# Kernel optimization log

Measured on AMD Instinct MI355X. Metric: run time of the kernel, lower is better.

## Reference

```python
import jax, jax.numpy as jnp
import numpy as np

B, S, IN, OUT = 4, 2048, 4096, 4096


def setup_inputs() -> dict:
    key = jax.random.key(0)
    kx, kw, kb = jax.random.split(key, 3)
    x = jax.random.randint(kx, (B, S, IN), -127, 128, dtype=jnp.int8)
    weight = jax.random.randint(kw, (OUT, IN), -127, 128, dtype=jnp.int8)
    # original module initializes bias to zeros(int32); use random int32 to exercise the add
    bias = jax.random.randint(kb, (1, OUT), -1000, 1000, dtype=jnp.int32)
    return {"x": x, "weight": weight, "bias": bias}


def reference(x, weight, bias):
    x_shape = x.shape
    x2 = x.reshape(-1, x_shape[-1])  # [tokens, IN], int8
    # dot_general with preferred_element_type=int32 -> int8 inputs, int32 accumulate
    y = jax.lax.dot_general(
        x2, weight,
        dimension_numbers=(((1,), (1,)), ((), ())),
        preferred_element_type=jnp.int32,
    )  # [tokens, OUT] int32
    y = y + bias  # broadcast [1, OUT] int32
    return y.reshape(*x_shape[:-1], -1)
```

## Files before the change

### kernel.cpp

```cpp
#include <hip/hip_runtime.h>
#include <stdint.h>

#define M_TOT 8192
#define N_TOT 4096
#define K_TOT 4096

typedef int v4i  __attribute__((ext_vector_type(4)));
typedef int v16i __attribute__((ext_vector_type(16)));

__device__ __forceinline__ void gload_lds16(const void* g, void* l) {
    __builtin_amdgcn_global_load_lds(
        (const __attribute__((address_space(1))) unsigned int*)g,
        (__attribute__((address_space(3))) unsigned int*)l,
        16, 0, 0);
}

#define WAIT_VMCNT0() __builtin_amdgcn_s_waitcnt(0x0f70)

__global__ __launch_bounds__(256) void pack_i32_to_i8(
        const int4* __restrict__ src, int* __restrict__ dst, int n4) {
    int idx = blockIdx.x * 1024 + threadIdx.x;
#pragma unroll
    for (int u = 0; u < 4; ++u, idx += 256) {
        const int4 a = src[idx];
        dst[idx] = (a.x & 255) | ((a.y & 255) << 8) |
                   ((a.z & 255) << 16) | (a.w << 24);
    }
}

__global__ __launch_bounds__(64, 1) void i8gemm_bias(
        const signed char* __restrict__ x,
        const signed char* __restrict__ w,
        const int* __restrict__ bias,
        int* __restrict__ out) {
    __shared__ __align__(16) signed char la[2][128 * 64];
    __shared__ __align__(16) signed char lb[2][128 * 64];

    const int lane = threadIdx.x;
    const int l31  = lane & 31;
    const int kh   = lane >> 5;
    const int bm0  = blockIdx.y * 128;
    const int bn0  = blockIdx.x * 128;

    int bv[4];
#pragma unroll
    for (int j = 0; j < 4; ++j) bv[j] = bias[bn0 + j * 32 + l31];
    v16i acc[4][4];
#pragma unroll
    for (int i = 0; i < 4; ++i)
#pragma unroll
        for (int j = 0; j < 4; ++j)
#pragma unroll
            for (int r = 0; r < 16; ++r) acc[i][j][r] = bv[j];

    const int fc = (lane & 3) ^ ((lane >> 3) & 3);
    const signed char* pa = x + (long)(bm0 + (lane >> 2)) * K_TOT + fc * 16;
    const signed char* pb = w + (long)(bn0 + (lane >> 2)) * K_TOT + fc * 16;

    const int swr = (l31 >> 1) & 3;

#pragma unroll
    for (int i = 0; i < 8; ++i) {
        gload_lds16(pa + (long)i * 16 * K_TOT, &la[0][i * 1024]);
        gload_lds16(pb + (long)i * 16 * K_TOT, &lb[0][i * 1024]);
    }

    for (int kt = 0; kt < K_TOT / 64; ++kt) {
        const int cur = kt & 1;
        const signed char* lac = la[cur];
        const signed char* lbc = lb[cur];

        WAIT_VMCNT0();
        __builtin_amdgcn_sched_barrier(0);

        v4i af[2][4], bf[2][4];
#pragma unroll
        for (int kk = 0; kk < 2; ++kk) {
            const int cs = ((kk * 2 + kh) ^ swr) * 16;
#pragma unroll
            for (int i = 0; i < 4; ++i) {
                af[kk][i] = *(const v4i*)(lac + (i * 32 + l31) * 64 + cs);
                bf[kk][i] = *(const v4i*)(lbc + (i * 32 + l31) * 64 + cs);
            }
        }
        __builtin_amdgcn_sched_barrier(0);

        if (kt + 1 < K_TOT / 64) {
            const long k0 = (long)(kt + 1) * 64;
            signed char* lan = la[cur ^ 1];
            signed char* lbn = lb[cur ^ 1];
#pragma unroll
            for (int i = 0; i < 8; ++i) {
                gload_lds16(pa + k0 + (long)i * 16 * K_TOT, lan + i * 1024);
                gload_lds16(pb + k0 + (long)i * 16 * K_TOT, lbn + i * 1024);
            }
        }
        __builtin_amdgcn_sched_barrier(0);

#pragma unroll
        for (int kk = 0; kk < 2; ++kk)
#pragma unroll
            for (int i = 0; i < 4; ++i)
#pragma unroll
                for (int j = 0; j < 4; ++j)
                    acc[i][j] = __builtin_amdgcn_mfma_i32_32x32x32_i8(
                        af[kk][i], bf[kk][j], acc[i][j], 0, 0, 0);
    }

#pragma unroll
    for (int i = 0; i < 4; ++i) {
        const int mbase = bm0 + i * 32 + 4 * kh;
#pragma unroll
        for (int j = 0; j < 4; ++j) {
            const int n = bn0 + j * 32 + l31;
#pragma unroll
            for (int r = 0; r < 16; ++r) {
                const int m = mbase + (r & 3) + 8 * (r >> 2);
                out[(long)m * N_TOT + n] = acc[i][j][r];
            }
        }
    }
}

extern "C" void kernel_launch(void* const* d_in, const int* in_sizes, int n_in,
                              void* d_out, int out_size, void* d_ws, size_t ws_size,
                              hipStream_t stream) {
    const int* x32  = (const int*)d_in[0];
    const int* w32  = (const int*)d_in[1];
    const int* bias = (const int*)d_in[2];
    int*       out  = (int*)d_out;

    signed char* xp = (signed char*)d_ws;
    signed char* wp = (signed char*)d_ws + (size_t)M_TOT * K_TOT;

    const int n4x = (M_TOT * K_TOT) / 4;
    const int n4w = (N_TOT * K_TOT) / 4;
    pack_i32_to_i8<<<n4x / 1024, 256, 0, stream>>>((const int4*)x32, (int*)xp, n4x);
    pack_i32_to_i8<<<n4w / 1024, 256, 0, stream>>>((const int4*)w32, (int*)wp, n4w);

    dim3 grid(N_TOT / 128, M_TOT / 128);
    i8gemm_bias<<<grid, 64, 0, stream>>>(xp, wp, bias, out);
}
```

Before: 420.8 us.

## Use 256x256 block tiles with four cooperating waves and swizzled block order

Grows the GEMM workgroup from one wave computing a 128x128 tile to four waves sharing a 256x256 tile. Each wave loads a quarter of the A and B panels into shared LDS and computes a 128x128 sub-tile. This halves global/L2 traffic per output and adds a block-index swizzle for L2 locality. The cost is a workgroup barrier every k-step, a 64KB LDS footprint, and fewer blocks (512) for 256 CUs.

```diff
diff --git a/kernel.cpp b/kernel.cpp
--- a/kernel.cpp
+++ b/kernel.cpp
@@ -28,23 +28,30 @@
     }
 }
 
-__global__ __launch_bounds__(64, 1) void i8gemm_bias(
+__global__ __launch_bounds__(256, 1) void i8gemm_bias(
         const signed char* __restrict__ x,
         const signed char* __restrict__ w,
         const int* __restrict__ bias,
         int* __restrict__ out) {
-    __shared__ __align__(16) signed char la[2][128 * 64];
-    __shared__ __align__(16) signed char lb[2][128 * 64];
+    __shared__ __align__(16) signed char la[2][256 * 64];
+    __shared__ __align__(16) signed char lb[2][256 * 64];
 
-    const int lane = threadIdx.x;
+    const int tid  = threadIdx.x;
+    const int lane = tid & 63;
+    const int wv   = tid >> 6;
     const int l31  = lane & 31;
     const int kh   = lane >> 5;
-    const int bm0  = blockIdx.y * 128;
-    const int bn0  = blockIdx.x * 128;
+    const int wr   = wv >> 1;
+    const int wc   = wv & 1;
+
+    const int flat = blockIdx.y * gridDim.x + blockIdx.x;
+    const int swz  = (flat & 7) * 64 + (flat >> 3);
+    const int bn0  = (swz & 15) * 256;
+    const int bm0  = (swz >> 4) * 256;
 
     int bv[4];
 #pragma unroll
-    for (int j = 0; j < 4; ++j) bv[j] = bias[bn0 + j * 32 + l31];
+    for (int j = 0; j < 4; ++j) bv[j] = bias[bn0 + wc * 128 + j * 32 + l31];
     v16i acc[4][4];
 #pragma unroll
     for (int i = 0; i < 4; ++i)
@@ -54,15 +61,16 @@
             for (int r = 0; r < 16; ++r) acc[i][j][r] = bv[j];
 
     const int fc = (lane & 3) ^ ((lane >> 3) & 3);
-    const signed char* pa = x + (long)(bm0 + (lane >> 2)) * K_TOT + fc * 16;
-    const signed char* pb = w + (long)(bn0 + (lane >> 2)) * K_TOT + fc * 16;
+    const signed char* pa = x + (long)(bm0 + wv * 64 + (lane >> 2)) * K_TOT + fc * 16;
+    const signed char* pb = w + (long)(bn0 + wv * 64 + (lane >> 2)) * K_TOT + fc * 16;
+    const int lbase = wv * 64 * 64;
 
     const int swr = (l31 >> 1) & 3;
 
 #pragma unroll
-    for (int i = 0; i < 8; ++i) {
-        gload_lds16(pa + (long)i * 16 * K_TOT, &la[0][i * 1024]);
-        gload_lds16(pb + (long)i * 16 * K_TOT, &lb[0][i * 1024]);
+    for (int i = 0; i < 4; ++i) {
+        gload_lds16(pa + (long)i * 16 * K_TOT, &la[0][lbase + i * 1024]);
+        gload_lds16(pb + (long)i * 16 * K_TOT, &lb[0][lbase + i * 1024]);
     }
 
     for (int kt = 0; kt < K_TOT / 64; ++kt) {
@@ -71,6 +79,7 @@
         const signed char* lbc = lb[cur];
 
         WAIT_VMCNT0();
+        __builtin_amdgcn_s_barrier();
         __builtin_amdgcn_sched_barrier(0);
 
         v4i af[2][4], bf[2][4];
@@ -79,18 +88,18 @@
             const int cs = ((kk * 2 + kh) ^ swr) * 16;
 #pragma unroll
             for (int i = 0; i < 4; ++i) {
-                af[kk][i] = *(const v4i*)(lac + (i * 32 + l31) * 64 + cs);
-                bf[kk][i] = *(const v4i*)(lbc + (i * 32 + l31) * 64 + cs);
+                af[kk][i] = *(const v4i*)(lac + (wr * 128 + i * 32 + l31) * 64 + cs);
+                bf[kk][i] = *(const v4i*)(lbc + (wc * 128 + i * 32 + l31) * 64 + cs);
             }
         }
         __builtin_amdgcn_sched_barrier(0);
 
         if (kt + 1 < K_TOT / 64) {
             const long k0 = (long)(kt + 1) * 64;
-            signed char* lan = la[cur ^ 1];
-            signed char* lbn = lb[cur ^ 1];
+            signed char* lan = la[cur ^ 1] + lbase;
+            signed char* lbn = lb[cur ^ 1] + lbase;
 #pragma unroll
-            for (int i = 0; i < 8; ++i) {
+            for (int i = 0; i < 4; ++i) {
                 gload_lds16(pa + k0 + (long)i * 16 * K_TOT, lan + i * 1024);
                 gload_lds16(pb + k0 + (long)i * 16 * K_TOT, lbn + i * 1024);
             }
@@ -109,10 +118,10 @@
 
 #pragma unroll
     for (int i = 0; i < 4; ++i) {
-        const int mbase = bm0 + i * 32 + 4 * kh;
+        const int mbase = bm0 + wr * 128 + i * 32 + 4 * kh;
 #pragma unroll
         for (int j = 0; j < 4; ++j) {
-            const int n = bn0 + j * 32 + l31;
+            const int n = bn0 + wc * 128 + j * 32 + l31;
 #pragma unroll
             for (int r = 0; r < 16; ++r) {
                 const int m = mbase + (r & 3) + 8 * (r >> 2);
@@ -138,6 +147,6 @@
     pack_i32_to_i8<<<n4x / 1024, 256, 0, stream>>>((const int4*)x32, (int*)xp, n4x);
     pack_i32_to_i8<<<n4w / 1024, 256, 0, stream>>>((const int4*)w32, (int*)wp, n4w);
 
-    dim3 grid(N_TOT / 128, M_TOT / 128);
-    i8gemm_bias<<<grid, 64, 0, stream>>>(xp, wp, bias, out);
+    dim3 grid(N_TOT / 256, M_TOT / 256);
+    i8gemm_bias<<<grid, 256, 0, stream>>>(xp, wp, bias, out);
 }
```

Result: no change. 418.0 us (-0.7%).
